# Kernel optimization log

Hardware: AMD Instinct MI355X
Metric: run time of the kernel (lower is better)

The kernel has to match this reference:

```python
import jax, jax.numpy as jnp
import numpy as np

TEMPERATURE = 30.0


def _adaptive_pool_28(sk):
    # sk: [b, 1, H, W] with H, W divisible by 28 -> [b, 1, 28, 28]
    b, c, h, w = sk.shape
    fh, fw = h // 28, w // 28
    return sk.reshape(b, c, 28, fh, 28, fw).mean(axis=(3, 5))


def setup_inputs() -> dict:
    key = jax.random.key(0)
    ks = jax.random.split(key, 6)
    bs, C, H, W, K = 8, 256, 64, 64, 16
    return {
        "x": jax.random.normal(ks[0], (bs, C, H, W), dtype=jnp.float32),
        "scene_knowledge": jax.random.normal(ks[1], (bs, 1, 56, 56), dtype=jnp.float32),
        "weight": jax.random.normal(ks[2], (K, C, C, 3, 3), dtype=jnp.float32) * 0.02,
        "bias": jax.random.normal(ks[3], (K, C), dtype=jnp.float32) * 0.02,
        "att_w1": jax.random.normal(ks[4], (196, 784), dtype=jnp.float32) * 0.05,
        "att_w2": jax.random.normal(ks[5], (16, 196), dtype=jnp.float32) * 0.05,
    }


def reference(x, scene_knowledge, weight, bias, att_w1, att_w2):
    bs, C, h, w = x.shape
    K = weight.shape[0]

    # ---- Attention: pooled scene knowledge -> softmax over K experts ----
    pooled = _adaptive_pool_28(scene_knowledge).reshape(bs, 28 * 28)  # [bs, 784]
    hdn = jax.nn.relu(pooled @ att_w1.T)                               # [bs, 196]
    logits = hdn @ att_w2.T                                            # [bs, K]
    att = jax.nn.softmax(logits / TEMPERATURE, axis=-1)                # [bs, K]

    # ---- Aggregate per-sample conv weights and biases ----
    agg_w = jnp.einsum("bk,koihw->boihw", att, weight)  # [bs, C, C, 3, 3]
    agg_b = att @ bias                                   # [bs, C]

    # ---- Per-sample conv (equivalent to groups=bs trick in torch) ----
    def per_sample_conv(xi, wi):
        # xi: [C, h, w], wi: [C, C, 3, 3]
        return jax.lax.conv_general_dilated(
            xi[None], wi, window_strides=(1, 1), padding="SAME",
            dimension_numbers=("NCHW", "OIHW", "NCHW"))[0]

    out = jax.vmap(per_sample_conv)(x, agg_w)            # [bs, C, h, w]
    out = out + agg_b[:, :, None, None] + x              # bias + residual
    return out
```

## Files before the change

kernel.cpp:

```cpp
#include <hip/hip_runtime.h>
#include <stdint.h>
#include <stddef.h>

typedef __bf16 bf16;
typedef __bf16 bf16x8 __attribute__((ext_vector_type(8)));
typedef __bf16 bf16x4 __attribute__((ext_vector_type(4)));
typedef float f32x4 __attribute__((ext_vector_type(4)));

static_assert(sizeof(bf16x8) == 16, "bf16x8 must be 16B");

__device__ __forceinline__ void gload_lds16(const void* g, void* l) {
    __builtin_amdgcn_global_load_lds(
        (const __attribute__((address_space(1))) uint32_t*)g,
        (__attribute__((address_space(3))) uint32_t*)l, 16, 0, 0);
}

__global__ void attn_kernel(const float* __restrict__ sk,
                            const float* __restrict__ w1,
                            const float* __restrict__ w2,
                            float* __restrict__ att) {
    const int b = blockIdx.x, t = threadIdx.x;
    __shared__ float pooled[784];
    __shared__ float hdn[196];
    __shared__ float logits[16];
    const float* skb = sk + (size_t)b * 3136;
    for (int e = t; e < 784; e += 256) {
        int oy = e / 28, ox = e % 28;
        const float* p = skb + (oy * 2) * 56 + ox * 2;
        pooled[e] = 0.25f * (p[0] + p[1] + p[56] + p[57]);
    }
    __syncthreads();
    if (t < 196) {
        float s = 0.f;
        const float* wr = w1 + (size_t)t * 784;
        for (int i = 0; i < 784; ++i) s += pooled[i] * wr[i];
        hdn[t] = s > 0.f ? s : 0.f;
    }
    __syncthreads();
    if (t < 16) {
        float s = 0.f;
        const float* wr = w2 + (size_t)t * 196;
        for (int j = 0; j < 196; ++j) s += hdn[j] * wr[j];
        logits[t] = s * (1.0f / 30.0f);
    }
    __syncthreads();
    if (t == 0) {
        float m = logits[0];
        for (int k = 1; k < 16; ++k) m = fmaxf(m, logits[k]);
        float e16[16], sum = 0.f;
        for (int k = 0; k < 16; ++k) { e16[k] = expf(logits[k] - m); sum += e16[k]; }
        float inv = 1.f / sum;
        for (int k = 0; k < 16; ++k) att[b * 16 + k] = e16[k] * inv;
    }
}

__global__ __launch_bounds__(256) void agg_kernel(
    const float* __restrict__ weight,
    const float* __restrict__ bias,
    const float* __restrict__ att,
    bf16* __restrict__ aggw,
    float* __restrict__ aggb) {
    const int bid = blockIdx.x;
    const int co = bid & 255, chunk = bid >> 8;
    const int t = threadIdx.x;

    __shared__ bf16 accW[8 * 576];

    if (chunk == 0 && t < 8) {
        float s = 0.f;
        for (int k = 0; k < 16; ++k) s += att[t * 16 + k] * bias[k * 256 + co];
        aggb[t * 256 + co] = s;
    }

    if (t < 144) {
        const float* wbase = weight + (size_t)co * 2304 + (size_t)chunk * 576 + (size_t)t * 4;
        float4 wv[16];
#pragma unroll
        for (int k = 0; k < 16; ++k)
            wv[k] = *(const float4*)(wbase + (size_t)k * 589824);
        float a[8][4];
#pragma unroll
        for (int b = 0; b < 8; ++b)
#pragma unroll
            for (int j = 0; j < 4; ++j) a[b][j] = 0.f;
#pragma unroll
        for (int k = 0; k < 16; ++k) {
#pragma unroll
            for (int b = 0; b < 8; ++b) {
                const float av = att[b * 16 + k];
                a[b][0] += av * wv[k].x;
                a[b][1] += av * wv[k].y;
                a[b][2] += av * wv[k].z;
                a[b][3] += av * wv[k].w;
            }
        }
#pragma unroll
        for (int b = 0; b < 8; ++b) {
            bf16x4 v;
#pragma unroll
            for (int j = 0; j < 4; ++j) v[j] = (bf16)a[b][j];
            *(bf16x4*)&accW[b * 576 + t * 4] = v;
        }
    }
    __syncthreads();

    const int half = co >> 7, co_l = co & 127;
    for (int s = t; s < 576; s += 256) {
        const int b = s / 72, r = s - b * 72;
        const int pos = r >> 3, cg = r & 7;
        bf16x8 v;
#pragma unroll
        for (int c = 0; c < 8; ++c) v[c] = accW[b * 576 + (cg * 8 + c) * 9 + pos];
        size_t o = (((((size_t)b * 9 + pos) * 4 + chunk) * 2 + half) * 8 + cg) * 128 + co_l;
        *(bf16x8*)(aggw + o * 8) = v;
    }
}

__global__ void transpose_kernel(const float* __restrict__ x, bf16* __restrict__ xt) {
    const int bid = blockIdx.x;
    const int b = bid >> 6, y = bid & 63;
    const int t = threadIdx.x;
    __shared__ bf16 T[256 * 64];
    const float* src = x + (size_t)b * 256 * 4096 + (size_t)y * 64;
    for (int i = 0; i < 16; ++i) {
        int v = t + 256 * i;
        int ci = v >> 4, x4 = (v & 15) * 4;
        float4 f = *(const float4*)(src + (size_t)ci * 4096 + x4);
        bf16* d = &T[ci * 64 + x4];
        d[0] = (bf16)f.x; d[1] = (bf16)f.y; d[2] = (bf16)f.z; d[3] = (bf16)f.w;
    }
    __syncthreads();
    bf16* dstb = xt + (size_t)bid * 16384;
    for (int i = 0; i < 8; ++i) {
        int c2 = t + 256 * i;
        int cg = c2 >> 6, xx = c2 & 63;
        bf16x8 v;
#pragma unroll
        for (int c = 0; c < 8; ++c) v[c] = T[(cg * 8 + c) * 64 + xx];
        *(bf16x8*)(dstb + (size_t)c2 * 8) = v;
    }
}

__global__ __launch_bounds__(256, 2) void conv_kernel(
    const bf16* __restrict__ xt, const bf16* __restrict__ aggw,
    const float* __restrict__ aggb, const float* __restrict__ xin,
    float* __restrict__ out) {
    const int bid = blockIdx.x;
    const int ytile = bid & 31;
    const int half = (bid >> 5) & 1;
    const int b = bid >> 6;
    const int tid = threadIdx.x;
    const int wave = tid >> 6, lane = tid & 63;
    const int wm = wave & 1, wn = wave >> 1;
    const int lane15 = lane & 15, quad = lane >> 4;

    __shared__ __align__(16) bf16 Xs[4][8][66][8];
    __shared__ __align__(16) bf16 Ws[8][128][8];

    f32x4 acc[4][4];
#pragma unroll
    for (int mt = 0; mt < 4; ++mt)
#pragma unroll
        for (int nt = 0; nt < 4; ++nt) acc[mt][nt] = f32x4{0.f, 0.f, 0.f, 0.f};

    {
        uint4 z; z.x = z.y = z.z = z.w = 0u;
        uint4* p = (uint4*)&Xs[0][0][0][0];
        for (int i = tid; i < 2112; i += 256) p[i] = z;
    }

    const int yrow = ytile * 2 - 1 + wave;
    const bool rowok = (yrow >= 0) && (yrow < 64);
    const bf16* xsrc = xt + ((size_t)b * 64 + (rowok ? yrow : 0)) * 16384 + (size_t)lane * 8;
    bf16* xdstbase = &Xs[wave][0][1][0];

    for (int chunk = 0; chunk < 4; ++chunk) {
        __syncthreads();
        if (rowok) {
            const bf16* s0 = xsrc + (size_t)chunk * 4096;
#pragma unroll
            for (int cg = 0; cg < 8; ++cg)
                gload_lds16(s0 + cg * 512, xdstbase + cg * 528);
        }
        const bf16* wchunkbase = aggw + (((size_t)b * 36 + chunk) * 2 + half) * 8192;
        for (int pos = 0; pos < 9; ++pos) {
            if (pos) __syncthreads();
            const bf16* wsrc = wchunkbase + (size_t)pos * 65536 + wave * 2048 + (size_t)lane * 8;
            bf16* wdst = ((bf16*)Ws) + wave * 2048;
#pragma unroll
            for (int i = 0; i < 4; ++i)
                gload_lds16(wsrc + i * 512, wdst + i * 512);
            __syncthreads();
            const int kh = pos / 3, kw = pos - kh * 3;
            const int xr = wn + kh;
#pragma unroll
            for (int s = 0; s < 2; ++s) {
                const int cg = s * 4 + quad;
                bf16x8 afr[4], bfr[4];
#pragma unroll
                for (int mt = 0; mt < 4; ++mt)
                    afr[mt] = *(const bf16x8*)&Ws[cg][wm * 64 + mt * 16 + lane15][0];
#pragma unroll
                for (int nt = 0; nt < 4; ++nt)
                    bfr[nt] = *(const bf16x8*)&Xs[xr][cg][kw + nt * 16 + lane15][0];
#pragma unroll
                for (int mt = 0; mt < 4; ++mt)
#pragma unroll
                    for (int nt = 0; nt < 4; ++nt)
                        acc[mt][nt] = __builtin_amdgcn_mfma_f32_16x16x32_bf16(
                            afr[mt], bfr[nt], acc[mt][nt], 0, 0, 0);
            }
        }
    }

    const int y = ytile * 2 + wn;
#pragma unroll
    for (int mt = 0; mt < 4; ++mt) {
#pragma unroll
        for (int r = 0; r < 4; ++r) {
            const int co = half * 128 + wm * 64 + mt * 16 + quad * 4 + r;
            const float bbv = aggb[b * 256 + co];
            const size_t rowbase = (((size_t)b * 256 + co) * 64 + y) * 64;
#pragma unroll
            for (int nt = 0; nt < 4; ++nt) {
                const size_t oidx = rowbase + nt * 16 + lane15;
                out[oidx] = acc[mt][nt][r] + bbv + xin[oidx];
            }
        }
    }
}

extern "C" void kernel_launch(void* const* d_in, const int* in_sizes, int n_in,
                              void* d_out, int out_size, void* d_ws, size_t ws_size,
                              hipStream_t stream) {
    const float* x    = (const float*)d_in[0];
    const float* sk   = (const float*)d_in[1];
    const float* wgt  = (const float*)d_in[2];
    const float* bias = (const float*)d_in[3];
    const float* w1   = (const float*)d_in[4];
    const float* w2   = (const float*)d_in[5];
    float* out = (float*)d_out;

    char* ws = (char*)d_ws;
    float* att  = (float*)(ws + 0);
    float* aggb = (float*)(ws + 1024);
    bf16*  aggw = (bf16*)(ws + 16384);
    bf16*  xt   = (bf16*)(ws + 16384 + 9437184);

    attn_kernel<<<8, 256, 0, stream>>>(sk, w1, w2, att);
    agg_kernel<<<1024, 256, 0, stream>>>(wgt, bias, att, aggw, aggb);
    transpose_kernel<<<512, 256, 0, stream>>>(x, xt);
    conv_kernel<<<512, 256, 0, stream>>>(xt, aggw, aggb, x, out);
}
```

Baseline: 189.9 us.

## Prefetch conv weights into registers, double-buffer input rows, enlarge spatial tile

The conv kernel now computes four output rows per block instead of two, which halves the grid and doubles reuse of each weight fragment. Weight fragments are loaded straight from global memory into registers, one kernel position ahead of use, instead of being staged through LDS with a barrier pair per position. Input rows for the next channel chunk are staged into a second LDS buffer while the current chunk is being computed. In exchange, register pressure roughly doubles (launch bounds drop to one block per SM, 32 accumulators plus two sets of weight fragments), and with only 256 blocks there is less latency hiding from occupancy.

```diff
diff --git a/kernel.cpp b/kernel.cpp
--- a/kernel.cpp
+++ b/kernel.cpp
@@ -141,90 +141,103 @@
     }
 }
 
-__global__ __launch_bounds__(256, 2) void conv_kernel(
+__global__ __launch_bounds__(256, 1) void conv_kernel(
     const bf16* __restrict__ xt, const bf16* __restrict__ aggw,
     const float* __restrict__ aggb, const float* __restrict__ xin,
     float* __restrict__ out) {
     const int bid = blockIdx.x;
-    const int ytile = bid & 31;
-    const int half = (bid >> 5) & 1;
-    const int b = bid >> 6;
+    const int ytile = bid & 15;
+    const int half = (bid >> 4) & 1;
+    const int b = bid >> 5;
     const int tid = threadIdx.x;
     const int wave = tid >> 6, lane = tid & 63;
     const int wm = wave & 1, wn = wave >> 1;
     const int lane15 = lane & 15, quad = lane >> 4;
 
-    __shared__ __align__(16) bf16 Xs[4][8][66][8];
-    __shared__ __align__(16) bf16 Ws[8][128][8];
-
-    f32x4 acc[4][4];
+    __shared__ __align__(16) bf16 Xs[2][6][8][66][8];
+
+    f32x4 acc[4][8];
 #pragma unroll
     for (int mt = 0; mt < 4; ++mt)
 #pragma unroll
-        for (int nt = 0; nt < 4; ++nt) acc[mt][nt] = f32x4{0.f, 0.f, 0.f, 0.f};
+        for (int nt = 0; nt < 8; ++nt) acc[mt][nt] = f32x4{0.f, 0.f, 0.f, 0.f};
 
     {
         uint4 z; z.x = z.y = z.z = z.w = 0u;
-        uint4* p = (uint4*)&Xs[0][0][0][0];
-        for (int i = tid; i < 2112; i += 256) p[i] = z;
-    }
-
-    const int yrow = ytile * 2 - 1 + wave;
-    const bool rowok = (yrow >= 0) && (yrow < 64);
-    const bf16* xsrc = xt + ((size_t)b * 64 + (rowok ? yrow : 0)) * 16384 + (size_t)lane * 8;
-    bf16* xdstbase = &Xs[wave][0][1][0];
-
-    for (int chunk = 0; chunk < 4; ++chunk) {
-        __syncthreads();
-        if (rowok) {
-            const bf16* s0 = xsrc + (size_t)chunk * 4096;
-#pragma unroll
-            for (int cg = 0; cg < 8; ++cg)
-                gload_lds16(s0 + cg * 512, xdstbase + cg * 528);
-        }
-        const bf16* wchunkbase = aggw + (((size_t)b * 36 + chunk) * 2 + half) * 8192;
-        for (int pos = 0; pos < 9; ++pos) {
-            if (pos) __syncthreads();
-            const bf16* wsrc = wchunkbase + (size_t)pos * 65536 + wave * 2048 + (size_t)lane * 8;
-            bf16* wdst = ((bf16*)Ws) + wave * 2048;
-#pragma unroll
-            for (int i = 0; i < 4; ++i)
-                gload_lds16(wsrc + i * 512, wdst + i * 512);
-            __syncthreads();
-            const int kh = pos / 3, kw = pos - kh * 3;
-            const int xr = wn + kh;
-#pragma unroll
-            for (int s = 0; s < 2; ++s) {
-                const int cg = s * 4 + quad;
-                bf16x8 afr[4], bfr[4];
-#pragma unroll
-                for (int mt = 0; mt < 4; ++mt)
-                    afr[mt] = *(const bf16x8*)&Ws[cg][wm * 64 + mt * 16 + lane15][0];
-#pragma unroll
-                for (int nt = 0; nt < 4; ++nt)
-                    bfr[nt] = *(const bf16x8*)&Xs[xr][cg][kw + nt * 16 + lane15][0];
-#pragma unroll
-                for (int mt = 0; mt < 4; ++mt)
-#pragma unroll
-                    for (int nt = 0; nt < 4; ++nt)
-                        acc[mt][nt] = __builtin_amdgcn_mfma_f32_16x16x32_bf16(
-                            afr[mt], bfr[nt], acc[mt][nt], 0, 0, 0);
-            }
-        }
-    }
-
-    const int y = ytile * 2 + wn;
+        uint4* p = (uint4*)&Xs[0][0][0][0][0];
+        for (int i = tid; i < 6336; i += 256) p[i] = z;
+    }
+    __syncthreads();
+
+    bf16x8 afr[2][8];
+    auto loadA = [&](int par, int chunk, int pos) {
+        const bf16* ab = aggw + ((((size_t)b * 9 + pos) * 4 + chunk) * 2 + half) * 8192;
+#pragma unroll
+        for (int s = 0; s < 2; ++s)
+#pragma unroll
+            for (int mt = 0; mt < 4; ++mt)
+                afr[par][s * 4 + mt] = *(const bf16x8*)(
+                    ab + ((size_t)((s * 4 + quad) * 128 + wm * 64 + mt * 16 + lane15)) * 8);
+    };
+    auto stageX = [&](int chunk, int buf) {
+#pragma unroll
+        for (int j = 0; j < 12; ++j) {
+            const int i = wave + 4 * j;
+            const int row = i >> 3, cg2 = i & 7;
+            const int yin = ytile * 4 - 1 + row;
+            if (yin >= 0 && yin < 64) {
+                const bf16* src = xt + (((size_t)b * 64 + yin) * 32 + chunk * 8 + cg2) * 512
+                                  + (size_t)lane * 8;
+                gload_lds16(src, &Xs[buf][row][cg2][1][0]);
+            }
+        }
+    };
+
+    loadA(0, 0, 0);
+    stageX(0, 0);
+    __syncthreads();
+
+#pragma unroll
+    for (int t = 0; t < 36; ++t) {
+        const int chunk = t / 9, pos = t % 9;
+        const int par = t & 1, xb = chunk & 1;
+        if (t < 35) loadA(par ^ 1, (t + 1) / 9, (t + 1) % 9);
+        if (pos == 0 && chunk < 3) stageX(chunk + 1, xb ^ 1);
+        const int kh = pos / 3, kw = pos % 3;
+#pragma unroll
+        for (int s = 0; s < 2; ++s) {
+            const int cg = s * 4 + quad;
+            bf16x8 bfr[8];
+#pragma unroll
+            for (int nt = 0; nt < 8; ++nt) {
+                const int rin = 2 * wn + (nt >> 2) + kh;
+                const int col = kw + (nt & 3) * 16 + lane15;
+                bfr[nt] = *(const bf16x8*)&Xs[xb][rin][cg][col][0];
+            }
+#pragma unroll
+            for (int mt = 0; mt < 4; ++mt)
+#pragma unroll
+                for (int nt = 0; nt < 8; ++nt)
+                    acc[mt][nt] = __builtin_amdgcn_mfma_f32_16x16x32_bf16(
+                        afr[par][s * 4 + mt], bfr[nt], acc[mt][nt], 0, 0, 0);
+        }
+        if (pos == 8 && chunk < 3) __syncthreads();
+    }
+
+    const int y0 = ytile * 4;
 #pragma unroll
     for (int mt = 0; mt < 4; ++mt) {
 #pragma unroll
         for (int r = 0; r < 4; ++r) {
             const int co = half * 128 + wm * 64 + mt * 16 + quad * 4 + r;
             const float bbv = aggb[b * 256 + co];
-            const size_t rowbase = (((size_t)b * 256 + co) * 64 + y) * 64;
-#pragma unroll
-            for (int nt = 0; nt < 4; ++nt) {
-                const size_t oidx = rowbase + nt * 16 + lane15;
-                out[oidx] = acc[mt][nt][r] + bbv + xin[oidx];
+            const size_t cb = ((size_t)b * 256 + co) * 4096;
+#pragma unroll
+            for (int nt = 0; nt < 8; ++nt) {
+                const int y = y0 + 2 * wn + (nt >> 2);
+                const int x = (nt & 3) * 16 + lane15;
+                const size_t o = cb + (size_t)y * 64 + x;
+                out[o] = acc[mt][nt][r] + bbv + xin[o];
             }
         }
     }
@@ -250,5 +263,5 @@
     attn_kernel<<<8, 256, 0, stream>>>(sk, w1, w2, att);
     agg_kernel<<<1024, 256, 0, stream>>>(wgt, bias, att, aggw, aggb);
     transpose_kernel<<<512, 256, 0, stream>>>(x, xt);
-    conv_kernel<<<512, 256, 0, stream>>>(xt, aggw, aggb, x, out);
-}
+    conv_kernel<<<256, 256, 0, stream>>>(xt, aggw, aggb, x, out);
+}
```

Result: slower. 211.6 us (+11.4%).

## Double-buffer conv weight tiles and merge attention with input transpose kernel

Applied to the files above, without the earlier changes.

The conv kernel now double-buffers the per-position weight tile in LDS, prefetching the next tile with async global-to-LDS loads while MFMAs run on the current one. This drops one barrier per position and hides load latency. Separately, the attention and transpose kernels are merged into one launch, removing a launch and letting the small attention blocks run alongside the transpose. The cost is doubled Ws LDS use (occupancy at 2 blocks/CU should still fit), and the merged prep kernel now allocates the 32KB transpose buffer in every block.

```diff
diff --git a/kernel.cpp b/kernel.cpp
--- a/kernel.cpp
+++ b/kernel.cpp
@@ -15,42 +15,69 @@
         (__attribute__((address_space(3))) uint32_t*)l, 16, 0, 0);
 }
 
-__global__ void attn_kernel(const float* __restrict__ sk,
+__global__ void prep_kernel(const float* __restrict__ x, bf16* __restrict__ xt,
+                            const float* __restrict__ sk,
                             const float* __restrict__ w1,
                             const float* __restrict__ w2,
                             float* __restrict__ att) {
-    const int b = blockIdx.x, t = threadIdx.x;
+    __shared__ bf16 T[256 * 64];
     __shared__ float pooled[784];
     __shared__ float hdn[196];
     __shared__ float logits[16];
-    const float* skb = sk + (size_t)b * 3136;
-    for (int e = t; e < 784; e += 256) {
-        int oy = e / 28, ox = e % 28;
-        const float* p = skb + (oy * 2) * 56 + ox * 2;
-        pooled[e] = 0.25f * (p[0] + p[1] + p[56] + p[57]);
-    }
-    __syncthreads();
-    if (t < 196) {
-        float s = 0.f;
-        const float* wr = w1 + (size_t)t * 784;
-        for (int i = 0; i < 784; ++i) s += pooled[i] * wr[i];
-        hdn[t] = s > 0.f ? s : 0.f;
-    }
-    __syncthreads();
-    if (t < 16) {
-        float s = 0.f;
-        const float* wr = w2 + (size_t)t * 196;
-        for (int j = 0; j < 196; ++j) s += hdn[j] * wr[j];
-        logits[t] = s * (1.0f / 30.0f);
-    }
-    __syncthreads();
-    if (t == 0) {
-        float m = logits[0];
-        for (int k = 1; k < 16; ++k) m = fmaxf(m, logits[k]);
-        float e16[16], sum = 0.f;
-        for (int k = 0; k < 16; ++k) { e16[k] = expf(logits[k] - m); sum += e16[k]; }
-        float inv = 1.f / sum;
-        for (int k = 0; k < 16; ++k) att[b * 16 + k] = e16[k] * inv;
+    const int t = threadIdx.x;
+
+    if (blockIdx.x < 512) {
+        const int bid = blockIdx.x;
+        const int b = bid >> 6, y = bid & 63;
+        const float* src = x + (size_t)b * 256 * 4096 + (size_t)y * 64;
+        for (int i = 0; i < 16; ++i) {
+            int v = t + 256 * i;
+            int ci = v >> 4, x4 = (v & 15) * 4;
+            float4 f = *(const float4*)(src + (size_t)ci * 4096 + x4);
+            bf16* d = &T[ci * 64 + x4];
+            d[0] = (bf16)f.x; d[1] = (bf16)f.y; d[2] = (bf16)f.z; d[3] = (bf16)f.w;
+        }
+        __syncthreads();
+        bf16* dstb = xt + (size_t)bid * 16384;
+        for (int i = 0; i < 8; ++i) {
+            int c2 = t + 256 * i;
+            int cg = c2 >> 6, xx = c2 & 63;
+            bf16x8 v;
+#pragma unroll
+            for (int c = 0; c < 8; ++c) v[c] = T[(cg * 8 + c) * 64 + xx];
+            *(bf16x8*)(dstb + (size_t)c2 * 8) = v;
+        }
+    } else {
+        const int b = blockIdx.x - 512;
+        const float* skb = sk + (size_t)b * 3136;
+        for (int e = t; e < 784; e += 256) {
+            int oy = e / 28, ox = e % 28;
+            const float* p = skb + (oy * 2) * 56 + ox * 2;
+            pooled[e] = 0.25f * (p[0] + p[1] + p[56] + p[57]);
+        }
+        __syncthreads();
+        if (t < 196) {
+            float s = 0.f;
+            const float* wr = w1 + (size_t)t * 784;
+            for (int i = 0; i < 784; ++i) s += pooled[i] * wr[i];
+            hdn[t] = s > 0.f ? s : 0.f;
+        }
+        __syncthreads();
+        if (t < 16) {
+            float s = 0.f;
+            const float* wr = w2 + (size_t)t * 196;
+            for (int j = 0; j < 196; ++j) s += hdn[j] * wr[j];
+            logits[t] = s * (1.0f / 30.0f);
+        }
+        __syncthreads();
+        if (t == 0) {
+            float m = logits[0];
+            for (int k = 1; k < 16; ++k) m = fmaxf(m, logits[k]);
+            float e16[16], sum = 0.f;
+            for (int k = 0; k < 16; ++k) { e16[k] = expf(logits[k] - m); sum += e16[k]; }
+            float inv = 1.f / sum;
+            for (int k = 0; k < 16; ++k) att[b * 16 + k] = e16[k] * inv;
+        }
     }
 }
 
@@ -113,31 +140,6 @@
         for (int c = 0; c < 8; ++c) v[c] = accW[b * 576 + (cg * 8 + c) * 9 + pos];
         size_t o = (((((size_t)b * 9 + pos) * 4 + chunk) * 2 + half) * 8 + cg) * 128 + co_l;
         *(bf16x8*)(aggw + o * 8) = v;
-    }
-}
-
-__global__ void transpose_kernel(const float* __restrict__ x, bf16* __restrict__ xt) {
-    const int bid = blockIdx.x;
-    const int b = bid >> 6, y = bid & 63;
-    const int t = threadIdx.x;
-    __shared__ bf16 T[256 * 64];
-    const float* src = x + (size_t)b * 256 * 4096 + (size_t)y * 64;
-    for (int i = 0; i < 16; ++i) {
-        int v = t + 256 * i;
-        int ci = v >> 4, x4 = (v & 15) * 4;
-        float4 f = *(const float4*)(src + (size_t)ci * 4096 + x4);
-        bf16* d = &T[ci * 64 + x4];
-        d[0] = (bf16)f.x; d[1] = (bf16)f.y; d[2] = (bf16)f.z; d[3] = (bf16)f.w;
-    }
-    __syncthreads();
-    bf16* dstb = xt + (size_t)bid * 16384;
-    for (int i = 0; i < 8; ++i) {
-        int c2 = t + 256 * i;
-        int cg = c2 >> 6, xx = c2 & 63;
-        bf16x8 v;
-#pragma unroll
-        for (int c = 0; c < 8; ++c) v[c] = T[(cg * 8 + c) * 64 + xx];
-        *(bf16x8*)(dstb + (size_t)c2 * 8) = v;
     }
 }
 
@@ -155,7 +157,7 @@
     const int lane15 = lane & 15, quad = lane >> 4;
 
     __shared__ __align__(16) bf16 Xs[4][8][66][8];
-    __shared__ __align__(16) bf16 Ws[8][128][8];
+    __shared__ __align__(16) bf16 Ws[2][8][128][8];
 
     f32x4 acc[4][4];
 #pragma unroll
@@ -168,29 +170,44 @@
         uint4* p = (uint4*)&Xs[0][0][0][0];
         for (int i = tid; i < 2112; i += 256) p[i] = z;
     }
+    __syncthreads();
 
     const int yrow = ytile * 2 - 1 + wave;
     const bool rowok = (yrow >= 0) && (yrow < 64);
     const bf16* xsrc = xt + ((size_t)b * 64 + (rowok ? yrow : 0)) * 16384 + (size_t)lane * 8;
     bf16* xdstbase = &Xs[wave][0][1][0];
 
-    for (int chunk = 0; chunk < 4; ++chunk) {
-        __syncthreads();
+    auto stageX = [&](int chunk) {
         if (rowok) {
             const bf16* s0 = xsrc + (size_t)chunk * 4096;
 #pragma unroll
             for (int cg = 0; cg < 8; ++cg)
                 gload_lds16(s0 + cg * 512, xdstbase + cg * 528);
         }
-        const bf16* wchunkbase = aggw + (((size_t)b * 36 + chunk) * 2 + half) * 8192;
+    };
+    auto loadW = [&](int chunk, int pos, int buf) {
+        const bf16* wsrc = aggw + ((((size_t)b * 9 + pos) * 4 + chunk) * 2 + half) * 8192
+                           + wave * 2048 + (size_t)lane * 8;
+        bf16* wdst = ((bf16*)Ws) + (size_t)buf * 8192 + wave * 2048;
+#pragma unroll
+        for (int i = 0; i < 4; ++i)
+            gload_lds16(wsrc + i * 512, wdst + i * 512);
+    };
+
+    stageX(0);
+    loadW(0, 0, 0);
+    __syncthreads();
+
+    for (int chunk = 0; chunk < 4; ++chunk) {
+#pragma unroll
         for (int pos = 0; pos < 9; ++pos) {
-            if (pos) __syncthreads();
-            const bf16* wsrc = wchunkbase + (size_t)pos * 65536 + wave * 2048 + (size_t)lane * 8;
-            bf16* wdst = ((bf16*)Ws) + wave * 2048;
-#pragma unroll
-            for (int i = 0; i < 4; ++i)
-                gload_lds16(wsrc + i * 512, wdst + i * 512);
-            __syncthreads();
+            const int par = (chunk + pos) & 1;
+            const bool last = (chunk == 3) && (pos == 8);
+            if (!last) {
+                const int nc = (pos == 8) ? chunk + 1 : chunk;
+                const int np = (pos == 8) ? 0 : pos + 1;
+                loadW(nc, np, par ^ 1);
+            }
             const int kh = pos / 3, kw = pos - kh * 3;
             const int xr = wn + kh;
 #pragma unroll
@@ -199,7 +216,7 @@
                 bf16x8 afr[4], bfr[4];
 #pragma unroll
                 for (int mt = 0; mt < 4; ++mt)
-                    afr[mt] = *(const bf16x8*)&Ws[cg][wm * 64 + mt * 16 + lane15][0];
+                    afr[mt] = *(const bf16x8*)&Ws[par][cg][wm * 64 + mt * 16 + lane15][0];
 #pragma unroll
                 for (int nt = 0; nt < 4; ++nt)
                     bfr[nt] = *(const bf16x8*)&Xs[xr][cg][kw + nt * 16 + lane15][0];
@@ -209,6 +226,13 @@
                     for (int nt = 0; nt < 4; ++nt)
                         acc[mt][nt] = __builtin_amdgcn_mfma_f32_16x16x32_bf16(
                             afr[mt], bfr[nt], acc[mt][nt], 0, 0, 0);
+            }
+            if (!last) {
+                __syncthreads();
+                if (pos == 8) {
+                    stageX(chunk + 1);
+                    __syncthreads();
+                }
             }
         }
     }
@@ -247,8 +271,7 @@
     bf16*  aggw = (bf16*)(ws + 16384);
     bf16*  xt   = (bf16*)(ws + 16384 + 9437184);
 
-    attn_kernel<<<8, 256, 0, stream>>>(sk, w1, w2, att);
+    prep_kernel<<<520, 256, 0, stream>>>(x, xt, sk, w1, w2, att);
     agg_kernel<<<1024, 256, 0, stream>>>(wgt, bias, att, aggw, aggb);
-    transpose_kernel<<<512, 256, 0, stream>>>(x, xt);
     conv_kernel<<<512, 256, 0, stream>>>(xt, aggw, aggb, x, out);
 }
```

After: 203.3 us. +7.0%, slower.
